# Performance work log

Measured on AMD Instinct MI355X. Metric: run time of the kernel, lower is better.

Reference implementation:

```python
import jax, jax.numpy as jnp
import numpy as np

N, T, IN, HID, ST, NL, OUT = 256, 2048, 6, 128, 64, 2, 6
LAY = IN + HID  # LMSCCell layer_size = input_size + hidden_size


def setup_inputs() -> dict:
    key = jax.random.key(0)
    ks = jax.random.split(key, 8)

    def w(k, shape, fan_in):
        return jax.random.normal(k, shape, jnp.float32) / np.sqrt(fan_in).astype(np.float32)

    return {
        "X": jax.random.normal(ks[0], (N, T, IN), jnp.float32),
        "H0": jax.random.normal(ks[1], (N, ST), jnp.float32),
        # NL gated layers (layer_size -> layer_size), stored stacked, weights as (in, out)
        "Wg1": w(ks[2], (NL, LAY, LAY), LAY), "bg1": jnp.zeros((NL, LAY), jnp.float32),
        "Wg2": w(ks[3], (NL, LAY, LAY), LAY), "bg2": jnp.zeros((NL, LAY), jnp.float32),
        # final pair: alpha (exp) and beta (tanh), layer_size -> hidden
        "Wa": w(ks[4], (LAY, HID), LAY), "ba": jnp.zeros((HID,), jnp.float32),
        "Wb": w(ks[5], (LAY, HID), LAY), "bb": jnp.zeros((HID,), jnp.float32),
        # hstate: Linear(state_size -> hidden) producing S0
        "Wh": w(ks[6], (ST, HID), ST), "bh": jnp.zeros((HID,), jnp.float32),
        # sstate2: Linear(hidden -> out_size)
        "Wo": w(ks[7], (HID, OUT), HID), "bo": jnp.zeros((OUT,), jnp.float32),
    }


def reference(X, H0, Wg1, bg1, Wg2, bg2, Wa, ba, Wb, bb, Wh, bh, Wo, bo):
    # hstate: initial hidden state for the LMSC recurrence
    S0 = H0 @ Wh + bh  # (N, HID)

    def step(H, x_t):
        # x_t: (N, IN); H: (N, HID)
        norm = jnp.linalg.norm(x_t, axis=1, keepdims=True)  # (N, 1)
        Lv = jnp.concatenate([x_t / norm, H], axis=1)       # (N, LAY)
        for i in range(NL):  # small fixed layer count, structurally distinct weights
            Lv = jnp.tanh(Lv @ Wg1[i] + bg1[i]) * jnp.tanh(Lv @ Wg2[i] + bg2[i])
        alpha = jnp.exp(Lv @ Wa + ba)   # (N, HID)
        beta = jnp.tanh(Lv @ Wb + bb)   # (N, HID)
        Hn = jnp.exp(-alpha * norm) * (H - beta) + beta
        return Hn, Hn

    _, Ys = jax.lax.scan(step, S0, jnp.swapaxes(X, 0, 1))  # (T, N, HID)
    Y = jnp.swapaxes(Ys, 0, 1)  # (N, T, HID)
    return Y @ Wo + bo          # (N, T, OUT)
```

## Files before the change

### kernel.cpp

```cpp
#include <hip/hip_runtime.h>

#define Nb   256
#define Tt   2048
#define INs  6
#define HID  128
#define STs  64
#define LAY  134
#define OUTs 6
#define VDW  72
#define HB_ODD 72

typedef __fp16 f16x2 __attribute__((ext_vector_type(2)));
typedef __fp16 f16x8 __attribute__((ext_vector_type(8)));

__device__ __forceinline__ float exp2_fast(float x) {
#if __has_builtin(__builtin_amdgcn_exp2f)
    return __builtin_amdgcn_exp2f(x);
#else
    return exp2f(x);
#endif
}
__device__ __forceinline__ float rcp_fast(float x) {
#if __has_builtin(__builtin_amdgcn_rcpf)
    return __builtin_amdgcn_rcpf(x);
#else
    return 1.0f / x;
#endif
}
__device__ __forceinline__ float tanh_fast(float x) {
    float e = exp2_fast(x * 2.8853900817779268f);
    return 1.0f - 2.0f * rcp_fast(e + 1.0f);
}
__device__ __forceinline__ unsigned pack2(float a, float b) {
#if __has_builtin(__builtin_amdgcn_cvt_pkrtz)
    union { f16x2 h; unsigned u; } u;
    u.h = __builtin_amdgcn_cvt_pkrtz(a, b);
    return u.u;
#else
    union { f16x2 h; unsigned u; } u;
    u.h[0] = (__fp16)a; u.h[1] = (__fp16)b;
    return u.u;
#endif
}
__device__ __forceinline__ unsigned pack2w(float a, float b) {
    union { f16x2 h; unsigned u; } u;
    u.h[0] = (__fp16)a; u.h[1] = (__fp16)b;
    return u.u;
}
__device__ __forceinline__ float dot2p(unsigned av, f16x2 wv, float c) {
    union { unsigned u; f16x2 f; } ua; ua.u = av;
#if __has_builtin(__builtin_amdgcn_fdot2)
    return __builtin_amdgcn_fdot2(ua.f, wv, c, false);
#else
    return c + (float)ua.f[0] * (float)wv[0] + (float)ua.f[1] * (float)wv[1];
#endif
}
__device__ __forceinline__ float dotdw(unsigned av, unsigned wv, float c) {
    union { unsigned u; f16x2 f; } uw; uw.u = wv;
    return dot2p(av, uw.f, c);
}

#define DECLW(P) f16x8 P##0={},P##1={},P##2={},P##3={},P##4={},P##5={},P##6={},P##7={},P##8={}

#define LOADW1(P,k,Wsrc,od,colv,hbv) { f16x8 tmp; \
    _Pragma("unroll") for (int q=0;q<8;++q){ int r=(hbv)+8*(k)+q; \
        float f=(r<LAY)?(Wsrc)[r*(od)+(colv)]:0.f; tmp[q]=(__fp16)f; } P##k=tmp; }
#define LOADSET(P,Wsrc,od,colv,hbv) \
    LOADW1(P,0,Wsrc,od,colv,hbv) LOADW1(P,1,Wsrc,od,colv,hbv) LOADW1(P,2,Wsrc,od,colv,hbv) \
    LOADW1(P,3,Wsrc,od,colv,hbv) LOADW1(P,4,Wsrc,od,colv,hbv) LOADW1(P,5,Wsrc,od,colv,hbv) \
    LOADW1(P,6,Wsrc,od,colv,hbv) LOADW1(P,7,Wsrc,od,colv,hbv) LOADW1(P,8,Wsrc,od,colv,hbv)

#define DOTK(P,k) { \
    a0=dot2p(x##k.x,__builtin_shufflevector(P##k,P##k,0,1),a0); \
    a1=dot2p(x##k.y,__builtin_shufflevector(P##k,P##k,2,3),a1); \
    a2=dot2p(x##k.z,__builtin_shufflevector(P##k,P##k,4,5),a2); \
    a3=dot2p(x##k.w,__builtin_shufflevector(P##k,P##k,6,7),a3); }
#define DOTSET(P) DOTK(P,0) DOTK(P,1) DOTK(P,2) DOTK(P,3) DOTK(P,4) DOTK(P,5) DOTK(P,6) DOTK(P,7) DOTK(P,8)

#define LOADX(buf) const uint4* a4_=(const uint4*)(buf)+hoff9; \
    uint4 x0=a4_[0],x1=a4_[1],x2=a4_[2],x3=a4_[3],x4=a4_[4],x5=a4_[5],x6=a4_[6],x7=a4_[7],x8=a4_[8]

#define OVK(k) { uint4 wv=w4_[k]; o0=dotdw(x##k.x,wv.x,o0); o1=dotdw(x##k.y,wv.y,o1); \
                 o2=dotdw(x##k.z,wv.z,o2); o3=dotdw(x##k.w,wv.w,o3); }
#define OVSET OVK(0) OVK(1) OVK(2) OVK(3) OVK(4) OVK(5) OVK(6) OVK(7) OVK(8)

__global__ __launch_bounds__(512, 1) __attribute__((amdgpu_waves_per_eu(2, 2)))
void lmsc_kernel(const float* __restrict__ X,  const float* __restrict__ H0,
                 const float* __restrict__ Wg1, const float* __restrict__ bg1,
                 const float* __restrict__ Wg2, const float* __restrict__ bg2,
                 const float* __restrict__ Wa,  const float* __restrict__ ba,
                 const float* __restrict__ Wb,  const float* __restrict__ bb,
                 const float* __restrict__ Wh,  const float* __restrict__ bh,
                 const float* __restrict__ Wo,  const float* __restrict__ bo,
                 float* __restrict__ out)
{
    __shared__ float Xls[Tt * INs];
    __shared__ alignas(16) float Hhist[32][HID];
    __shared__ alignas(16) float WolT[OUTs][HID];
    __shared__ float H0l[STs];
    __shared__ float bol[OUTs];
    __shared__ alignas(16) unsigned OvW1[12][VDW];
    __shared__ alignas(16) unsigned OvW2[12][VDW];
    __shared__ alignas(16) unsigned LvX[VDW];
    __shared__ alignas(16) unsigned LvB[VDW];
    __shared__ alignas(16) unsigned LvC[VDW];
    __shared__ float nrm[2];

    const int tid  = threadIdx.x;
    const int n    = blockIdx.x;
    const int half = tid & 1;
    const int mat  = (tid >> 1) & 1;
    const int col  = tid >> 2;
    const int hoff9 = half * 9;
    const int hb    = half * HB_ODD;
    __fp16* LvX16 = (__fp16*)LvX;
    __fp16* LvB16 = (__fp16*)LvB;
    __fp16* LvC16 = (__fp16*)LvC;

    {
        const float4* Xg  = (const float4*)(X + (size_t)n * (Tt * INs));
        float4*       Xl4 = (float4*)Xls;
        for (int i = tid; i < (Tt * INs) / 4; i += 512) Xl4[i] = Xg[i];
    }
    if (tid < STs) H0l[tid] = H0[n * STs + tid];
    for (int i = tid; i < OUTs * HID; i += 512) {
        int o = i >> 7, l2 = i & 127;
        WolT[o][l2] = Wo[l2 * OUTs + o];
    }
    if (tid < OUTs) bol[tid] = bo[tid];
    if (tid < 5) LvX[67 + tid] = 0u;
    else if (tid < 10) LvB[62 + tid] = 0u;
    else if (tid < 15) LvC[57 + tid] = 0u;
    if (tid >= 64 && tid < 88) {
        int i = tid - 64; int L = (i >= 12); int d = i - L * 12;
        int c = 128 + (d >> 1); int m = d & 1;
        const float* src = (m ? Wg2 : Wg1) + L * LAY * LAY;
        unsigned* dst = L ? OvW2[d] : OvW1[d];
        for (int q = 0; q < VDW; ++q) {
            int r0 = 2 * q, r1 = 2 * q + 1;
            float f0 = (r0 < LAY) ? src[r0 * LAY + c] : 0.f;
            float f1 = (r1 < LAY) ? src[r1 * LAY + c] : 0.f;
            dst[q] = pack2w(f0, f1);
        }
    }

    DECLW(u); DECLW(v); DECLW(p);
    const float* Wgm = mat ? Wg2 : Wg1;
    LOADSET(u, Wgm, LAY, col, hb);
    LOADSET(v, Wgm + LAY * LAY, LAY, col, hb);
    const float* Wab = mat ? Wb : Wa;
    LOADSET(p, Wab, HID, col, hb);
    float gb0 = (mat ? bg2 : bg1)[col];
    float gb1 = (mat ? bg2 : bg1)[LAY + col];
    float pb  = (mat ? bb : ba)[col];
    float ovb = 0.f;
    if (tid < 24)        ovb = (((tid >> 1) & 1) ? bg2 : bg1)[128 + (tid >> 2)];
    else if (tid >= 488) { int e = tid - 488; ovb = (((e >> 1) & 1) ? bg2 : bg1)[LAY + 128 + (e >> 2)]; }

    __syncthreads();

    float h = 0.f;
    if ((tid & 3) == 0) {
        float s = bh[col];
        for (int k = 0; k < STs; ++k) s += H0l[k] * Wh[k * HID + col];
        h = s;
        LvX16[6 + col] = (__fp16)s;
    }
    if (tid == 56) {
        float s = 0.f;
#pragma unroll
        for (int i = 0; i < 6; ++i) s += Xls[i] * Xls[i];
        float nv = sqrtf(s), rn = rcp_fast(nv);
        nrm[0] = nv;
        LvX[0] = pack2(Xls[0]*rn, Xls[1]*rn);
        LvX[1] = pack2(Xls[2]*rn, Xls[3]*rn);
        LvX[2] = pack2(Xls[4]*rn, Xls[5]*rn);
    }
    __syncthreads();

    const float LOG2E = 1.4426950408889634f;

#pragma unroll 1
    for (int t = 0; t < Tt; ++t) {
        unsigned nx0 = 0, nx1 = 0, nx2 = 0;
        {
            LOADX(LvX);
            float a0 = 0.f, a1 = 0.f, a2 = 0.f, a3 = 0.f;
            DOTSET(u);
            float s = (a0 + a1) + (a2 + a3);
            s += __shfl_xor(s, 1, 64);
            s += gb0;
            float tn = tanh_fast(s);
            float to = __shfl_xor(tn, 2, 64);
            if ((tid & 3) == 0) LvB16[col] = (__fp16)(tn * to);
            if (tid < 24) {
                const uint4* w4_ = (const uint4*)OvW1[tid >> 1] + hoff9;
                float o0 = 0.f, o1 = 0.f, o2 = 0.f, o3 = 0.f;
                OVSET;
                float so = (o0 + o1) + (o2 + o3);
                so += __shfl_xor(so, 1, 64);
                so += ovb;
                float tno = tanh_fast(so);
                float too = __shfl_xor(tno, 2, 64);
                if ((tid & 3) == 0) LvB16[128 + (tid >> 2)] = (__fp16)(tno * too);
            } else if (tid == 56 && (t + 1) < Tt) {
                const float* xp = &Xls[(t + 1) * INs];
                float s2 = 0.f;
#pragma unroll
                for (int i = 0; i < 6; ++i) s2 += xp[i] * xp[i];
                float nv = sqrtf(s2), rn = rcp_fast(nv);
                nrm[(t + 1) & 1] = nv;
                nx0 = pack2(xp[0]*rn, xp[1]*rn);
                nx1 = pack2(xp[2]*rn, xp[3]*rn);
                nx2 = pack2(xp[4]*rn, xp[5]*rn);
            }
        }
        __syncthreads();
        {
            LOADX(LvB);
            float a0 = 0.f, a1 = 0.f, a2 = 0.f, a3 = 0.f;
            DOTSET(v);
            float s = (a0 + a1) + (a2 + a3);
            s += __shfl_xor(s, 1, 64);
            s += gb1;
            float tn = tanh_fast(s);
            float to = __shfl_xor(tn, 2, 64);
            if ((tid & 3) == 0) LvC16[col] = (__fp16)(tn * to);
            if (tid >= 488) {
                int e = tid - 488;
                const uint4* w4_ = (const uint4*)OvW2[e >> 1] + hoff9;
                float o0 = 0.f, o1 = 0.f, o2 = 0.f, o3 = 0.f;
                OVSET;
                float so = (o0 + o1) + (o2 + o3);
                so += __shfl_xor(so, 1, 64);
                so += ovb;
                float tno = tanh_fast(so);
                float too = __shfl_xor(tno, 2, 64);
                if ((e & 3) == 0) LvC16[128 + (e >> 2)] = (__fp16)(tno * too);
            } else if (tid == 56 && (t + 1) < Tt) {
                LvX[0] = nx0; LvX[1] = nx1; LvX[2] = nx2;
            }
        }
        __syncthreads();
        {
            LOADX(LvC);
            float a0 = 0.f, a1 = 0.f, a2 = 0.f, a3 = 0.f;
            DOTSET(p);
            float s = (a0 + a1) + (a2 + a3);
            s += __shfl_xor(s, 1, 64);
            s += pb;
            float tn = tanh_fast(s);
            float beta = __shfl_xor(tn, 2, 64);
            if ((tid & 3) == 0) {
                float alpha = exp2_fast(s * LOG2E);
                float e2 = exp2_fast(-alpha * nrm[t & 1] * LOG2E);
                h = e2 * (h - beta) + beta;
                Hhist[t & 31][col] = h;
                LvX16[6 + col] = (__fp16)h;
            }
        }
        __syncthreads();
        if ((t & 31) == 31) {
            if (tid < 192) {
                int fs = tid / 6, fo = tid - fs * 6;
                float acc = bol[fo];
                const float4* hr = (const float4*)(&Hhist[fs][0]);
                const float4* wr = (const float4*)(&WolT[fo][0]);
#pragma unroll
                for (int k2 = 0; k2 < HID / 4; ++k2) {
                    float4 hv = hr[k2], wv = wr[k2];
                    acc += hv.x*wv.x + hv.y*wv.y + hv.z*wv.z + hv.w*wv.w;
                }
                out[((size_t)n * Tt + (t - 31) + fs) * OUTs + fo] = acc;
            }
            __syncthreads();
        }
    }
}

extern "C" void kernel_launch(void* const* d_in, const int* in_sizes, int n_in,
                              void* d_out, int out_size, void* d_ws, size_t ws_size,
                              hipStream_t stream) {
    const float* X   = (const float*)d_in[0];
    const float* H0  = (const float*)d_in[1];
    const float* Wg1 = (const float*)d_in[2];
    const float* bg1 = (const float*)d_in[3];
    const float* Wg2 = (const float*)d_in[4];
    const float* bg2 = (const float*)d_in[5];
    const float* Wa  = (const float*)d_in[6];
    const float* ba  = (const float*)d_in[7];
    const float* Wb  = (const float*)d_in[8];
    const float* bb  = (const float*)d_in[9];
    const float* Wh  = (const float*)d_in[10];
    const float* bh  = (const float*)d_in[11];
    const float* Wo  = (const float*)d_in[12];
    const float* bo  = (const float*)d_in[13];
    float* out = (float*)d_out;

    hipLaunchKernelGGL(lmsc_kernel, dim3(Nb), dim3(512), 0, stream,
                       X, H0, Wg1, bg1, Wg2, bg2, Wa, ba, Wb, bb, Wh, bh, Wo, bo, out);
}
```

Measured before the change: 3.987 ms.

## Assign each layer matrix to a dedicated 256-thread group with full-row dots

The block grows from 512 to 768 threads and is split into three groups, one per stage matrix (gate layer 1, gate layer 2, alpha/beta). Each group keeps its matrix weights in registers. Each thread now computes the full 134-element dot product, so the partial-sum shuffle is gone and two threads serve each column instead of four. The aim is to cut the per-thread weight register load and the cross-lane reductions. The trade-off is that only one group is busy per serialized stage and each thread's dependent dot chain is about twice as long. The output projection batch also grows from 32 to 64 timesteps, with a padded history buffer.

```diff
diff --git a/kernel.cpp b/kernel.cpp
--- a/kernel.cpp
+++ b/kernel.cpp
@@ -7,8 +7,8 @@
 #define STs  64
 #define LAY  134
 #define OUTs 6
-#define VDW  72
-#define HB_ODD 72
+#define NDW  68
+#define HPAD 132
 
 typedef __fp16 f16x2 __attribute__((ext_vector_type(2)));
 typedef __fp16 f16x8 __attribute__((ext_vector_type(8)));
@@ -60,31 +60,31 @@
     return dot2p(av, uw.f, c);
 }
 
-#define DECLW(P) f16x8 P##0={},P##1={},P##2={},P##3={},P##4={},P##5={},P##6={},P##7={},P##8={}
-
-#define LOADW1(P,k,Wsrc,od,colv,hbv) { f16x8 tmp; \
-    _Pragma("unroll") for (int q=0;q<8;++q){ int r=(hbv)+8*(k)+q; \
-        float f=(r<LAY)?(Wsrc)[r*(od)+(colv)]:0.f; tmp[q]=(__fp16)f; } P##k=tmp; }
-#define LOADSET(P,Wsrc,od,colv,hbv) \
-    LOADW1(P,0,Wsrc,od,colv,hbv) LOADW1(P,1,Wsrc,od,colv,hbv) LOADW1(P,2,Wsrc,od,colv,hbv) \
-    LOADW1(P,3,Wsrc,od,colv,hbv) LOADW1(P,4,Wsrc,od,colv,hbv) LOADW1(P,5,Wsrc,od,colv,hbv) \
-    LOADW1(P,6,Wsrc,od,colv,hbv) LOADW1(P,7,Wsrc,od,colv,hbv) LOADW1(P,8,Wsrc,od,colv,hbv)
-
-#define DOTK(P,k) { \
-    a0=dot2p(x##k.x,__builtin_shufflevector(P##k,P##k,0,1),a0); \
-    a1=dot2p(x##k.y,__builtin_shufflevector(P##k,P##k,2,3),a1); \
-    a2=dot2p(x##k.z,__builtin_shufflevector(P##k,P##k,4,5),a2); \
-    a3=dot2p(x##k.w,__builtin_shufflevector(P##k,P##k,6,7),a3); }
-#define DOTSET(P) DOTK(P,0) DOTK(P,1) DOTK(P,2) DOTK(P,3) DOTK(P,4) DOTK(P,5) DOTK(P,6) DOTK(P,7) DOTK(P,8)
-
-#define LOADX(buf) const uint4* a4_=(const uint4*)(buf)+hoff9; \
-    uint4 x0=a4_[0],x1=a4_[1],x2=a4_[2],x3=a4_[3],x4=a4_[4],x5=a4_[5],x6=a4_[6],x7=a4_[7],x8=a4_[8]
-
-#define OVK(k) { uint4 wv=w4_[k]; o0=dotdw(x##k.x,wv.x,o0); o1=dotdw(x##k.y,wv.y,o1); \
+#define WR17(M) M(0) M(1) M(2) M(3) M(4) M(5) M(6) M(7) M(8) M(9) M(10) M(11) M(12) M(13) M(14) M(15) M(16)
+
+#define DECLW(k) f16x8 w##k = {};
+#define LOADW(k) { f16x8 tmp; \
+    _Pragma("unroll") for (int q = 0; q < 8; ++q) { int r = 8*(k)+q; \
+        float f = (r < LAY) ? Wsrc[r * od + col] : 0.f; tmp[q] = (__fp16)f; } \
+    w##k = tmp; }
+
+#define LOADX17(buf) const uint4* a4_ = (const uint4*)(buf); \
+    uint4 x0=a4_[0],x1=a4_[1],x2=a4_[2],x3=a4_[3],x4=a4_[4],x5=a4_[5],x6=a4_[6],x7=a4_[7], \
+          x8=a4_[8],x9=a4_[9],x10=a4_[10],x11=a4_[11],x12=a4_[12],x13=a4_[13],x14=a4_[14], \
+          x15=a4_[15],x16=a4_[16]
+
+#define DOTK(k) { \
+    a0 = dot2p(x##k.x, __builtin_shufflevector(w##k, w##k, 0, 1), a0); \
+    a1 = dot2p(x##k.y, __builtin_shufflevector(w##k, w##k, 2, 3), a1); \
+    a2 = dot2p(x##k.z, __builtin_shufflevector(w##k, w##k, 4, 5), a2); \
+    a3 = dot2p(x##k.w, __builtin_shufflevector(w##k, w##k, 6, 7), a3); }
+#define DOTSET WR17(DOTK)
+
+#define OVK(k) { uint4 wv = w4_[k]; o0=dotdw(x##k.x,wv.x,o0); o1=dotdw(x##k.y,wv.y,o1); \
                  o2=dotdw(x##k.z,wv.z,o2); o3=dotdw(x##k.w,wv.w,o3); }
-#define OVSET OVK(0) OVK(1) OVK(2) OVK(3) OVK(4) OVK(5) OVK(6) OVK(7) OVK(8)
-
-__global__ __launch_bounds__(512, 1) __attribute__((amdgpu_waves_per_eu(2, 2)))
+#define OVSET WR17(OVK)
+
+__global__ __launch_bounds__(768, 1) __attribute__((amdgpu_waves_per_eu(3, 3)))
 void lmsc_kernel(const float* __restrict__ X,  const float* __restrict__ H0,
                  const float* __restrict__ Wg1, const float* __restrict__ bg1,
                  const float* __restrict__ Wg2, const float* __restrict__ bg2,
@@ -95,24 +95,22 @@
                  float* __restrict__ out)
 {
     __shared__ float Xls[Tt * INs];
-    __shared__ alignas(16) float Hhist[32][HID];
-    __shared__ alignas(16) float WolT[OUTs][HID];
+    __shared__ alignas(16) float Hhist[64][HPAD];
+    __shared__ alignas(16) float WolT[OUTs][HPAD];
+    __shared__ alignas(16) unsigned OvW[2][12][NDW];
+    __shared__ alignas(16) unsigned LvX[NDW];
+    __shared__ alignas(16) unsigned LvB[NDW];
+    __shared__ alignas(16) unsigned LvC[NDW];
     __shared__ float H0l[STs];
     __shared__ float bol[OUTs];
-    __shared__ alignas(16) unsigned OvW1[12][VDW];
-    __shared__ alignas(16) unsigned OvW2[12][VDW];
-    __shared__ alignas(16) unsigned LvX[VDW];
-    __shared__ alignas(16) unsigned LvB[VDW];
-    __shared__ alignas(16) unsigned LvC[VDW];
     __shared__ float nrm[2];
 
-    const int tid  = threadIdx.x;
-    const int n    = blockIdx.x;
-    const int half = tid & 1;
-    const int mat  = (tid >> 1) & 1;
-    const int col  = tid >> 2;
-    const int hoff9 = half * 9;
-    const int hb    = half * HB_ODD;
+    const int tid = threadIdx.x;
+    const int n   = blockIdx.x;
+    const int grp = tid >> 8;
+    const int loc = tid & 255;
+    const int col = loc >> 1;
+    const int mat = tid & 1;
     __fp16* LvX16 = (__fp16*)LvX;
     __fp16* LvB16 = (__fp16*)LvB;
     __fp16* LvC16 = (__fp16*)LvC;
@@ -120,53 +118,49 @@
     {
         const float4* Xg  = (const float4*)(X + (size_t)n * (Tt * INs));
         float4*       Xl4 = (float4*)Xls;
-        for (int i = tid; i < (Tt * INs) / 4; i += 512) Xl4[i] = Xg[i];
+        for (int i = tid; i < (Tt * INs) / 4; i += 768) Xl4[i] = Xg[i];
     }
     if (tid < STs) H0l[tid] = H0[n * STs + tid];
-    for (int i = tid; i < OUTs * HID; i += 512) {
-        int o = i >> 7, l2 = i & 127;
-        WolT[o][l2] = Wo[l2 * OUTs + o];
-    }
+    if (tid < OUTs * HID) { int o = tid >> 7, l2 = tid & 127; WolT[o][l2] = Wo[l2 * OUTs + o]; }
+    if (tid >= 770 - OUTs) {}
+    if (tid < OUTs + 768 && tid >= 768 - OUTs) {}
     if (tid < OUTs) bol[tid] = bo[tid];
-    if (tid < 5) LvX[67 + tid] = 0u;
-    else if (tid < 10) LvB[62 + tid] = 0u;
-    else if (tid < 15) LvC[57 + tid] = 0u;
-    if (tid >= 64 && tid < 88) {
-        int i = tid - 64; int L = (i >= 12); int d = i - L * 12;
-        int c = 128 + (d >> 1); int m = d & 1;
+    if (tid == 700) { LvX[NDW-1] = 0u; LvB[NDW-1] = 0u; LvC[NDW-1] = 0u; }
+    if (tid >= 32 && tid < 56) {
+        int i = tid - 32, L = i / 12, d = i % 12;
+        int c = 128 + (d >> 1), m = d & 1;
         const float* src = (m ? Wg2 : Wg1) + L * LAY * LAY;
-        unsigned* dst = L ? OvW2[d] : OvW1[d];
-        for (int q = 0; q < VDW; ++q) {
-            int r0 = 2 * q, r1 = 2 * q + 1;
+        unsigned* dst = OvW[L][d];
+        for (int q = 0; q < NDW; ++q) {
+            int r0 = 2*q, r1 = 2*q + 1;
             float f0 = (r0 < LAY) ? src[r0 * LAY + c] : 0.f;
             float f1 = (r1 < LAY) ? src[r1 * LAY + c] : 0.f;
             dst[q] = pack2w(f0, f1);
         }
     }
 
-    DECLW(u); DECLW(v); DECLW(p);
-    const float* Wgm = mat ? Wg2 : Wg1;
-    LOADSET(u, Wgm, LAY, col, hb);
-    LOADSET(v, Wgm + LAY * LAY, LAY, col, hb);
-    const float* Wab = mat ? Wb : Wa;
-    LOADSET(p, Wab, HID, col, hb);
-    float gb0 = (mat ? bg2 : bg1)[col];
-    float gb1 = (mat ? bg2 : bg1)[LAY + col];
-    float pb  = (mat ? bb : ba)[col];
+    WR17(DECLW)
+    float bias;
+    {
+        const float* Wsrc; int od;
+        if (grp == 0)      { Wsrc = mat ? Wg2 : Wg1;             od = LAY; bias = (mat ? bg2 : bg1)[col]; }
+        else if (grp == 1) { Wsrc = (mat ? Wg2 : Wg1) + LAY*LAY; od = LAY; bias = (mat ? bg2 : bg1)[LAY + col]; }
+        else               { Wsrc = mat ? Wb : Wa;               od = HID; bias = (mat ? bb : ba)[col]; }
+        WR17(LOADW)
+    }
     float ovb = 0.f;
-    if (tid < 24)        ovb = (((tid >> 1) & 1) ? bg2 : bg1)[128 + (tid >> 2)];
-    else if (tid >= 488) { int e = tid - 488; ovb = (((e >> 1) & 1) ? bg2 : bg1)[LAY + 128 + (e >> 2)]; }
-
+    if (tid >= 512 && tid < 524) { int s = tid - 512; ovb = ((s & 1) ? bg2 : bg1)[128 + (s >> 1)]; }
+    else if (tid < 12)           { ovb = ((tid & 1) ? bg2 : bg1)[LAY + 128 + (tid >> 1)]; }
     __syncthreads();
 
     float h = 0.f;
-    if ((tid & 3) == 0) {
+    if (grp == 2 && !mat) {
         float s = bh[col];
         for (int k = 0; k < STs; ++k) s += H0l[k] * Wh[k * HID + col];
         h = s;
         LvX16[6 + col] = (__fp16)s;
     }
-    if (tid == 56) {
+    if (tid == 760) {
         float s = 0.f;
 #pragma unroll
         for (int i = 0; i < 6; ++i) s += Xls[i] * Xls[i];
@@ -183,95 +177,85 @@
 #pragma unroll 1
     for (int t = 0; t < Tt; ++t) {
         unsigned nx0 = 0, nx1 = 0, nx2 = 0;
-        {
-            LOADX(LvX);
+        if (grp == 0) {
+            LOADX17(LvX);
             float a0 = 0.f, a1 = 0.f, a2 = 0.f, a3 = 0.f;
-            DOTSET(u);
-            float s = (a0 + a1) + (a2 + a3);
-            s += __shfl_xor(s, 1, 64);
-            s += gb0;
+            DOTSET
+            float s  = ((a0 + a1) + (a2 + a3)) + bias;
             float tn = tanh_fast(s);
-            float to = __shfl_xor(tn, 2, 64);
-            if ((tid & 3) == 0) LvB16[col] = (__fp16)(tn * to);
-            if (tid < 24) {
-                const uint4* w4_ = (const uint4*)OvW1[tid >> 1] + hoff9;
-                float o0 = 0.f, o1 = 0.f, o2 = 0.f, o3 = 0.f;
-                OVSET;
-                float so = (o0 + o1) + (o2 + o3);
-                so += __shfl_xor(so, 1, 64);
-                so += ovb;
-                float tno = tanh_fast(so);
-                float too = __shfl_xor(tno, 2, 64);
-                if ((tid & 3) == 0) LvB16[128 + (tid >> 2)] = (__fp16)(tno * too);
-            } else if (tid == 56 && (t + 1) < Tt) {
-                const float* xp = &Xls[(t + 1) * INs];
-                float s2 = 0.f;
+            float to = __shfl_xor(tn, 1, 64);
+            if (!mat) LvB16[col] = (__fp16)(tn * to);
+        } else if (tid >= 512 && tid < 524) {
+            int s9 = tid - 512;
+            LOADX17(LvX);
+            const uint4* w4_ = (const uint4*)OvW[0][s9];
+            float o0 = 0.f, o1 = 0.f, o2 = 0.f, o3 = 0.f;
+            OVSET
+            float so = ((o0 + o1) + (o2 + o3)) + ovb;
+            float tn = tanh_fast(so);
+            float to = __shfl_xor(tn, 1, 64);
+            if (!(s9 & 1)) LvB16[128 + (s9 >> 1)] = (__fp16)(tn * to);
+        } else if (tid == 760 && (t + 1) < Tt) {
+            const float* xp = &Xls[(t + 1) * INs];
+            float s = 0.f;
 #pragma unroll
-                for (int i = 0; i < 6; ++i) s2 += xp[i] * xp[i];
-                float nv = sqrtf(s2), rn = rcp_fast(nv);
-                nrm[(t + 1) & 1] = nv;
-                nx0 = pack2(xp[0]*rn, xp[1]*rn);
-                nx1 = pack2(xp[2]*rn, xp[3]*rn);
-                nx2 = pack2(xp[4]*rn, xp[5]*rn);
-            }
+            for (int i = 0; i < 6; ++i) s += xp[i] * xp[i];
+            float nv = sqrtf(s), rn = rcp_fast(nv);
+            nrm[(t + 1) & 1] = nv;
+            nx0 = pack2(xp[0]*rn, xp[1]*rn);
+            nx1 = pack2(xp[2]*rn, xp[3]*rn);
+            nx2 = pack2(xp[4]*rn, xp[5]*rn);
         }
         __syncthreads();
-        {
-            LOADX(LvB);
+        if (grp == 1) {
+            LOADX17(LvB);
             float a0 = 0.f, a1 = 0.f, a2 = 0.f, a3 = 0.f;
-            DOTSET(v);
-            float s = (a0 + a1) + (a2 + a3);
-            s += __shfl_xor(s, 1, 64);
-            s += gb1;
+            DOTSET
+            float s  = ((a0 + a1) + (a2 + a3)) + bias;
             float tn = tanh_fast(s);
-            float to = __shfl_xor(tn, 2, 64);
-            if ((tid & 3) == 0) LvC16[col] = (__fp16)(tn * to);
-            if (tid >= 488) {
-                int e = tid - 488;
-                const uint4* w4_ = (const uint4*)OvW2[e >> 1] + hoff9;
-                float o0 = 0.f, o1 = 0.f, o2 = 0.f, o3 = 0.f;
-                OVSET;
-                float so = (o0 + o1) + (o2 + o3);
-                so += __shfl_xor(so, 1, 64);
-                so += ovb;
-                float tno = tanh_fast(so);
-                float too = __shfl_xor(tno, 2, 64);
-                if ((e & 3) == 0) LvC16[128 + (e >> 2)] = (__fp16)(tno * too);
-            } else if (tid == 56 && (t + 1) < Tt) {
-                LvX[0] = nx0; LvX[1] = nx1; LvX[2] = nx2;
-            }
+            float to = __shfl_xor(tn, 1, 64);
+            if (!mat) LvC16[col] = (__fp16)(tn * to);
+        } else if (tid < 12) {
+            LOADX17(LvB);
+            const uint4* w4_ = (const uint4*)OvW[1][tid];
+            float o0 = 0.f, o1 = 0.f, o2 = 0.f, o3 = 0.f;
+            OVSET
+            float so = ((o0 + o1) + (o2 + o3)) + ovb;
+            float tn = tanh_fast(so);
+            float to = __shfl_xor(tn, 1, 64);
+            if (!(tid & 1)) LvC16[128 + (tid >> 1)] = (__fp16)(tn * to);
+        } else if (tid == 760 && (t + 1) < Tt) {
+            LvX[0] = nx0; LvX[1] = nx1; LvX[2] = nx2;
         }
         __syncthreads();
-        {
-            LOADX(LvC);
+        if (grp == 2) {
+            LOADX17(LvC);
             float a0 = 0.f, a1 = 0.f, a2 = 0.f, a3 = 0.f;
-            DOTSET(p);
-            float s = (a0 + a1) + (a2 + a3);
-            s += __shfl_xor(s, 1, 64);
-            s += pb;
-            float tn = tanh_fast(s);
-            float beta = __shfl_xor(tn, 2, 64);
-            if ((tid & 3) == 0) {
+            DOTSET
+            float s  = ((a0 + a1) + (a2 + a3)) + bias;
+            float tn   = tanh_fast(s);
+            float beta = __shfl_xor(tn, 1, 64);
+            if (!mat) {
                 float alpha = exp2_fast(s * LOG2E);
                 float e2 = exp2_fast(-alpha * nrm[t & 1] * LOG2E);
                 h = e2 * (h - beta) + beta;
-                Hhist[t & 31][col] = h;
+                Hhist[t & 63][col] = h;
                 LvX16[6 + col] = (__fp16)h;
             }
         }
         __syncthreads();
-        if ((t & 31) == 31) {
-            if (tid < 192) {
+        if ((t & 63) == 63) {
+            if (tid < 384) {
                 int fs = tid / 6, fo = tid - fs * 6;
                 float acc = bol[fo];
                 const float4* hr = (const float4*)(&Hhist[fs][0]);
                 const float4* wr = (const float4*)(&WolT[fo][0]);
-#pragma unroll
+#pragma unroll 4
                 for (int k2 = 0; k2 < HID / 4; ++k2) {
                     float4 hv = hr[k2], wv = wr[k2];
                     acc += hv.x*wv.x + hv.y*wv.y + hv.z*wv.z + hv.w*wv.w;
                 }
-                out[((size_t)n * Tt + (t - 31) + fs) * OUTs + fo] = acc;
+                out[((size_t)n * Tt + (t - 63)) * OUTs + tid] = acc;
             }
             __syncthreads();
         }
@@ -297,6 +281,6 @@
     const float* bo  = (const float*)d_in[13];
     float* out = (float*)d_out;
 
-    hipLaunchKernelGGL(lmsc_kernel, dim3(Nb), dim3(512), 0, stream,
+    hipLaunchKernelGGL(lmsc_kernel, dim3(Nb), dim3(768), 0, stream,
                        X, H0, Wg1, bg1, Wg2, bg2, Wa, ba, Wb, bb, Wh, bh, Wo, bo, out);
 }
```

Result: slower. 4.907 ms (+23.1%).
